# Kernel tuning notes

Measured on AMD Instinct MI355X. Metric: run time of the kernel, lower is better.

## Reference

```python
import jax, jax.numpy as jnp
from jax import lax
import numpy as np

PATCH = 8


def setup_inputs() -> dict:
    key = jax.random.key(0)
    ks = jax.random.split(key, 6)
    B, C, H, W = 8, 128, 256, 256
    half = C // 2
    x = jax.random.normal(ks[0], (B, C, H, W), dtype=jnp.float32)
    # nn.Parameter(torch.randn(...)) -> unit normal real spectral filter
    fft_filt = jax.random.normal(ks[1], (C, PATCH, PATCH // 2 + 1), dtype=jnp.float32)
    w_in = jax.random.normal(ks[2], (C, C), dtype=jnp.float32) * 0.05
    w_before = jax.random.normal(ks[3], (half, half), dtype=jnp.float32) * 0.05
    w_dw = jax.random.normal(ks[4], (half, 1, 3, 3), dtype=jnp.float32) * 0.05
    w_out = jax.random.normal(ks[5], (C, half), dtype=jnp.float32) * 0.05
    return {"x": x, "fft_filt": fft_filt, "w_in": w_in,
            "w_before": w_before, "w_dw": w_dw, "w_out": w_out}


def reference(x, fft_filt, w_in, w_before, w_dw, w_out):
    B, C, H, W = x.shape
    p = PATCH
    pad_h = (p - H % p) % p
    pad_w = (p - W % p) % p
    xp = jnp.pad(x, ((0, 0), (0, 0), (0, pad_h), (0, pad_w))) if (pad_h or pad_w) else x
    Hp, Wp = H + pad_h, W + pad_w
    h, w = Hp // p, Wp // p

    # project_in: 1x1 conv, no bias
    y = jnp.einsum('bchw,oc->bohw', xp, w_in)

    # b c (h p1) (w p2) -> b h w c p1 p2
    yp = y.reshape(B, C, h, p, w, p).transpose(0, 2, 4, 1, 3, 5)
    yf = jnp.fft.rfft2(yp)                      # complex, last-two-axes FFT of 8x8 patches
    yf = yf * fft_filt                          # real filter broadcast over (b,h,w)
    yi = jnp.fft.irfft2(yf, s=(p, p))
    # b h w c p1 p2 -> b c (h p1) (w p2)
    y = yi.transpose(0, 3, 1, 4, 2, 5).reshape(B, C, Hp, Wp)

    # chunk + gated GELU (torch default gelu = exact erf)
    x1, x2 = jnp.split(y, 2, axis=1)
    g = jax.nn.gelu(x1, approximate=False) * x2

    # before_dwconv: 1x1 conv on half channels
    g = jnp.einsum('bchw,oc->bohw', g, w_before)
    # depthwise 3x3, padding 1
    g = lax.conv_general_dilated(g, w_dw, window_strides=(1, 1), padding='SAME',
                                 feature_group_count=C // 2,
                                 dimension_numbers=('NCHW', 'OIHW', 'NCHW'))
    # project_out: 1x1 conv half -> dim
    out = jnp.einsum('bchw,oc->bohw', g, w_out)
    out = out[:, :, :H, :W]
    return out + x
```

## Files before the change

### kernel.cpp

```cpp
#include <hip/hip_runtime.h>
#include <math.h>
#include <stdint.h>

#define BB 8
#define CC 128
#define HH 256
#define WW 256
#define PLANE (HH * WW)
#define YSTR 68

typedef __attribute__((ext_vector_type(8))) short short8;
typedef __attribute__((ext_vector_type(4))) float f32x4;
typedef __attribute__((ext_vector_type(2))) int i32x2;

__device__ __forceinline__ unsigned short f2bf(float f) {
  unsigned u = __float_as_uint(f);
  u += 0x7FFFu + ((u >> 16) & 1u);
  return (unsigned short)(u >> 16);
}
__device__ __forceinline__ float bf2f(unsigned short h) {
  return __uint_as_float(((unsigned)h) << 16);
}

__device__ __forceinline__ i32x2 tr16(uint32_t addr) {
  i32x2 d;
  asm volatile("ds_read_b64_tr_b16 %0, %1" : "=v"(d) : "v"(addr));
  return d;
}
__device__ __forceinline__ short8 mk8(i32x2 a, i32x2 b) {
  union { i32x2 d[2]; short8 s; } u;
  u.d[0] = a; u.d[1] = b;
  return u.s;
}

__global__ __launch_bounds__(256) void prep_kernel(
    const float* __restrict__ filt, const float* __restrict__ w_in,
    const float* __restrict__ w_before, const float* __restrict__ w_out,
    float* __restrict__ kkt, unsigned short* __restrict__ w_in_h,
    unsigned short* __restrict__ w_in_l,
    unsigned short* __restrict__ w_before_h,
    unsigned short* __restrict__ w_before_l, float* __restrict__ w_out_t) {
  int idx = blockIdx.x * 256 + threadIdx.x;
  if (idx < 8192) {
    int c = idx >> 6;
    int un = idx & 63;
    int u = un >> 3, n = un & 7;
    const float cs8[8] = {1.f,  0.70710678118654752f,  0.f, -0.70710678118654752f,
                          -1.f, -0.70710678118654752f, 0.f, 0.70710678118654752f};
    float s = 0.f;
#pragma unroll
    for (int p = 0; p < 8; ++p) {
#pragma unroll
      for (int q = 0; q < 5; ++q) {
        float m = (q == 0 || q == 4) ? 1.f : 2.f;
        s += m * filt[(c * 8 + p) * 5 + q] * cs8[(p * u + q * n) & 7];
      }
    }
    kkt[un * 128 + c] = s * (1.f / 64.f);
  } else if (idx < 24576) {
    int j = idx - 8192;
    float f = w_in[j];
    unsigned short h = f2bf(f);
    w_in_h[j] = h;
    w_in_l[j] = f2bf(f - bf2f(h));
  } else if (idx < 28672) {
    int j = idx - 24576;
    float f = w_before[j];
    unsigned short h = f2bf(f);
    w_before_h[j] = h;
    w_before_l[j] = f2bf(f - bf2f(h));
  } else if (idx < 36864) {
    int j = idx - 28672;
    int o = j >> 6, c = j & 63;
    w_out_t[c * 128 + o] = w_out[o * 64 + c];
  }
}

__global__ __launch_bounds__(256) void fused1_kernel(
    const float* __restrict__ x, const unsigned short* __restrict__ w_in_h,
    const unsigned short* __restrict__ w_in_l,
    const unsigned short* __restrict__ w_before_h,
    const unsigned short* __restrict__ w_before_l,
    const float* __restrict__ kkt, float* __restrict__ g2) {
  __shared__ __align__(16) char smem[51200];
  unsigned short* xh = (unsigned short*)smem;
  unsigned short* xl = (unsigned short*)(smem + 16384);
  float* yb = (float*)smem;
  unsigned short* gh = (unsigned short*)(smem + 34816);
  unsigned short* gl = (unsigned short*)(smem + 43008);

  int bid = blockIdx.x;
  int b = bid >> 10;
  int py = (bid >> 5) & 31;
  int pxb = bid & 31;
  int h0 = py * 8, w0 = pxb * 8;
  int t = threadIdx.x;
  const float* xb = x + (size_t)b * CC * PLANE;

#pragma unroll
  for (int it = 0; it < 4; ++it) {
    int oc = t + it * 256;
    int c = oc >> 3, ph = oc & 7;
    const float* src = xb + (size_t)c * PLANE + (size_t)(h0 + ph) * WW + w0;
    float4 v0 = *(const float4*)src;
    float4 v1 = *(const float4*)(src + 4);
    float v[8] = {v0.x, v0.y, v0.z, v0.w, v1.x, v1.y, v1.z, v1.w};
    unsigned hu[4], lu[4];
#pragma unroll
    for (int q = 0; q < 4; ++q) {
      unsigned short ha = f2bf(v[2 * q]), hb = f2bf(v[2 * q + 1]);
      unsigned short la = f2bf(v[2 * q] - bf2f(ha));
      unsigned short lb = f2bf(v[2 * q + 1] - bf2f(hb));
      hu[q] = (unsigned)ha | ((unsigned)hb << 16);
      lu[q] = (unsigned)la | ((unsigned)lb << 16);
    }
    int ks = c >> 5, wc = c & 31;
    int blk = (wc >> 2) & 1, sg = wc >> 3, jj = wc & 3;
    int nt = ph >> 1, colh = ph & 1;
    int e = ((ks * 4 + nt) * 2 + blk) * 256 + (sg * 4 + jj) * 16 + colh * 8;
    *(uint4*)(xh + e) = make_uint4(hu[0], hu[1], hu[2], hu[3]);
    *(uint4*)(xl + e) = make_uint4(lu[0], lu[1], lu[2], lu[3]);
  }
  __syncthreads();

  int l = t & 63;
  int wv = t >> 6;
  int l15 = l & 15, l4 = l >> 4;
  uint32_t trbase =
      (uint32_t)(uintptr_t)smem + (uint32_t)(l15 * 2 + l4 * 128);

  f32x4 zero4 = {0.f, 0.f, 0.f, 0.f};
  f32x4 acc[2][4];
#pragma unroll
  for (int mt = 0; mt < 2; ++mt)
#pragma unroll
    for (int nt = 0; nt < 4; ++nt) acc[mt][nt] = zero4;

#pragma unroll
  for (int ks = 0; ks < 4; ++ks) {
    short8 ah[2], al[2];
#pragma unroll
    for (int mt = 0; mt < 2; ++mt) {
      int o = wv * 32 + mt * 16 + l15;
      ah[mt] = *(const short8*)(w_in_h + o * 128 + ks * 32 + l4 * 8);
      al[mt] = *(const short8*)(w_in_l + o * 128 + ks * 32 + l4 * 8);
    }
#pragma unroll
    for (int nt = 0; nt < 4; ++nt) {
      uint32_t base = trbase + (uint32_t)((ks * 4 + nt) * 1024);
      i32x2 h0v = tr16(base);
      i32x2 h1v = tr16(base + 512);
      i32x2 l0v = tr16(base + 16384);
      i32x2 l1v = tr16(base + 16384 + 512);
      asm volatile("s_waitcnt lgkmcnt(0)" ::: "memory");
      __builtin_amdgcn_sched_barrier(0);
      short8 bh = mk8(h0v, h1v);
      short8 bl = mk8(l0v, l1v);
#pragma unroll
      for (int mt = 0; mt < 2; ++mt) {
        acc[mt][nt] = __builtin_amdgcn_mfma_f32_16x16x32_bf16(
            ah[mt], bh, acc[mt][nt], 0, 0, 0);
        acc[mt][nt] = __builtin_amdgcn_mfma_f32_16x16x32_bf16(
            ah[mt], bl, acc[mt][nt], 0, 0, 0);
        acc[mt][nt] = __builtin_amdgcn_mfma_f32_16x16x32_bf16(
            al[mt], bh, acc[mt][nt], 0, 0, 0);
      }
    }
  }
  __syncthreads();

#pragma unroll
  for (int mt = 0; mt < 2; ++mt)
#pragma unroll
    for (int nt = 0; nt < 4; ++nt)
#pragma unroll
      for (int r = 0; r < 4; ++r) {
        int o = wv * 32 + mt * 16 + l4 * 4 + r;
        yb[o * YSTR + nt * 16 + l15] = acc[mt][nt][r];
      }
  __syncthreads();

  int ob = t >> 3;
  int pb = t & 7;
  float acc2[4][8];
#pragma unroll
  for (int i = 0; i < 4; ++i)
#pragma unroll
    for (int j = 0; j < 8; ++j) acc2[i][j] = 0.f;

#pragma unroll
  for (int s = 0; s < 8; ++s) {
    int r = (pb - s) & 7;
    float yr[4][8];
#pragma unroll
    for (int i = 0; i < 4; ++i) {
      const float* p = yb + (ob * 4 + i) * YSTR + r * 8;
      float4 v0 = *(const float4*)p;
      float4 v1 = *(const float4*)(p + 4);
      yr[i][0] = v0.x; yr[i][1] = v0.y; yr[i][2] = v0.z; yr[i][3] = v0.w;
      yr[i][4] = v1.x; yr[i][5] = v1.y; yr[i][6] = v1.z; yr[i][7] = v1.w;
    }
#pragma unroll
    for (int tt = 0; tt < 8; ++tt) {
      float4 kv = *(const float4*)(kkt + (s * 8 + tt) * 128 + ob * 4);
      float ka[4] = {kv.x, kv.y, kv.z, kv.w};
#pragma unroll
      for (int i = 0; i < 4; ++i)
#pragma unroll
        for (int j = 0; j < 8; ++j)
          acc2[i][j] += ka[i] * yr[i][(j - tt) & 7];
    }
  }
  __syncthreads();

#pragma unroll
  for (int i = 0; i < 4; ++i) {
    float* dst = yb + (ob * 4 + i) * YSTR + pb * 8;
    *(float4*)dst = make_float4(acc2[i][0], acc2[i][1], acc2[i][2], acc2[i][3]);
    *(float4*)(dst + 4) =
        make_float4(acc2[i][4], acc2[i][5], acc2[i][6], acc2[i][7]);
  }
  __syncthreads();

#pragma unroll
  for (int it = 0; it < 2; ++it) {
    int oc = t + it * 256;
    int c = oc >> 3, ocl = oc & 7;
    const float* pa = yb + c * YSTR + ocl * 8;
    const float* pg = yb + (c + 64) * YSTR + ocl * 8;
    float4 a0 = *(const float4*)pa, a1 = *(const float4*)(pa + 4);
    float4 g0 = *(const float4*)pg, g1 = *(const float4*)(pg + 4);
    float av[8] = {a0.x, a0.y, a0.z, a0.w, a1.x, a1.y, a1.z, a1.w};
    float gv[8] = {g0.x, g0.y, g0.z, g0.w, g1.x, g1.y, g1.z, g1.w};
    unsigned hu[4], lu[4];
#pragma unroll
    for (int q = 0; q < 4; ++q) {
      float r0, r1;
      {
        float a = av[2 * q];
        r0 = 0.5f * a * (1.f + erff(a * 0.70710678118654752f)) * gv[2 * q];
      }
      {
        float a = av[2 * q + 1];
        r1 = 0.5f * a * (1.f + erff(a * 0.70710678118654752f)) * gv[2 * q + 1];
      }
      unsigned short ha = f2bf(r0), hb = f2bf(r1);
      unsigned short la = f2bf(r0 - bf2f(ha)), lb = f2bf(r1 - bf2f(hb));
      hu[q] = (unsigned)ha | ((unsigned)hb << 16);
      lu[q] = (unsigned)la | ((unsigned)lb << 16);
    }
    int ks = c >> 5, wc = c & 31;
    int blk = (wc >> 2) & 1, sg = wc >> 3, jj = wc & 3;
    int nt = ocl >> 1, colh = ocl & 1;
    int e = ((ks * 4 + nt) * 2 + blk) * 256 + (sg * 4 + jj) * 16 + colh * 8;
    *(uint4*)(gh + e) = make_uint4(hu[0], hu[1], hu[2], hu[3]);
    *(uint4*)(gl + e) = make_uint4(lu[0], lu[1], lu[2], lu[3]);
  }
  __syncthreads();

  f32x4 accd[4];
#pragma unroll
  for (int nt = 0; nt < 4; ++nt) accd[nt] = zero4;

  uint32_t gtrbase = (uint32_t)(uintptr_t)smem + 34816u +
                     (uint32_t)(l15 * 2 + l4 * 128);
#pragma unroll
  for (int ks = 0; ks < 2; ++ks) {
    int o = wv * 16 + l15;
    short8 wbh = *(const short8*)(w_before_h + o * 64 + ks * 32 + l4 * 8);
    short8 wbl = *(const short8*)(w_before_l + o * 64 + ks * 32 + l4 * 8);
#pragma unroll
    for (int nt = 0; nt < 4; ++nt) {
      uint32_t base = gtrbase + (uint32_t)((ks * 4 + nt) * 1024);
      i32x2 h0v = tr16(base);
      i32x2 h1v = tr16(base + 512);
      i32x2 l0v = tr16(base + 8192);
      i32x2 l1v = tr16(base + 8192 + 512);
      asm volatile("s_waitcnt lgkmcnt(0)" ::: "memory");
      __builtin_amdgcn_sched_barrier(0);
      short8 bh = mk8(h0v, h1v);
      short8 bl = mk8(l0v, l1v);
      accd[nt] =
          __builtin_amdgcn_mfma_f32_16x16x32_bf16(wbh, bh, accd[nt], 0, 0, 0);
      accd[nt] =
          __builtin_amdgcn_mfma_f32_16x16x32_bf16(wbh, bl, accd[nt], 0, 0, 0);
      accd[nt] =
          __builtin_amdgcn_mfma_f32_16x16x32_bf16(wbl, bh, accd[nt], 0, 0, 0);
    }
  }
#pragma unroll
  for (int nt = 0; nt < 4; ++nt)
#pragma unroll
    for (int r = 0; r < 4; ++r) {
      int o = wv * 16 + l4 * 4 + r;
      yb[o * YSTR + nt * 16 + l15] = accd[nt][r];
    }
  __syncthreads();

#pragma unroll
  for (int it = 0; it < 2; ++it) {
    int oc = t + it * 256;
    int o = oc >> 3, ocl = oc & 7;
    const float* p = yb + o * YSTR + ocl * 8;
    float4 v0 = *(const float4*)p;
    float4 v1 = *(const float4*)(p + 4);
    float* dst = g2 + (size_t)b * 64 * PLANE + (size_t)o * PLANE +
                 (size_t)(h0 + ocl) * WW + w0;
    *(float4*)dst = v0;
    *(float4*)(dst + 4) = v1;
  }
}

__global__ __launch_bounds__(256) void dwconv_kernel(
    const float* __restrict__ g2, const float* __restrict__ w_dw,
    float* __restrict__ dout) {
  int wseg = blockIdx.x;
  int hseg = blockIdx.y;
  int bc = blockIdx.z;
  int c = bc & 63;
  const float* src = g2 + (size_t)bc * PLANE;
  float* dst = dout + (size_t)bc * PLANE;
  __shared__ float tile[34][66];
  int w0 = wseg * 64, h0 = hseg * 32;
  int t = threadIdx.x;
  for (int f = t; f < 34 * 66; f += 256) {
    int r = f / 66, cl = f - r * 66;
    int hh = h0 + r - 1, ww = w0 + cl - 1;
    float v = 0.f;
    if (hh >= 0 && hh < HH && ww >= 0 && ww < WW) v = src[hh * WW + ww];
    tile[r][cl] = v;
  }
  float k9[9];
#pragma unroll
  for (int i = 0; i < 9; ++i) k9[i] = w_dw[c * 9 + i];
  __syncthreads();
  int cl = t & 63;
#pragma unroll
  for (int rep = 0; rep < 8; ++rep) {
    int r = rep * 4 + (t >> 6);
    float s = 0.f;
#pragma unroll
    for (int i = 0; i < 3; ++i)
#pragma unroll
      for (int j = 0; j < 3; ++j) s += k9[i * 3 + j] * tile[r + i][cl + j];
    dst[(size_t)(h0 + r) * WW + w0 + cl] = s;
  }
}

__global__ __launch_bounds__(256) void mixout_kernel(
    const float* __restrict__ d, const float* __restrict__ w_out_t,
    const float* __restrict__ x, float* __restrict__ out) {
  int bid = blockIdx.x;
  int wseg = bid & 3;
  int hh = (bid >> 2) & 255;
  int b = bid >> 10;
  __shared__ float ds[64 * 64];
  int t = threadIdx.x;
  const float* dbase = d + (size_t)b * 64 * PLANE + (size_t)hh * WW + wseg * 64;
#pragma unroll
  for (int i = 0; i < 4; ++i) {
    int f = t + 256 * i;
    int c = f >> 4, k4 = f & 15;
    *(float4*)(ds + c * 64 + k4 * 4) =
        *(const float4*)(dbase + (size_t)c * PLANE + k4 * 4);
  }
  __syncthreads();

  int og = __builtin_amdgcn_readfirstlane(t >> 6);
  int pix = t & 63;
  float acc[32];
#pragma unroll
  for (int i = 0; i < 32; ++i) acc[i] = 0.f;

  const float* wt = w_out_t + og * 32;
#pragma unroll 2
  for (int c = 0; c < 64; ++c) {
    float xv = ds[c * 64 + pix];
#pragma unroll
    for (int i = 0; i < 32; ++i) acc[i] += wt[c * 128 + i] * xv;
  }

  size_t pbase =
      (size_t)b * CC * PLANE + (size_t)hh * WW + (size_t)wseg * 64 + pix;
#pragma unroll
  for (int i = 0; i < 32; ++i) {
    int o = og * 32 + i;
    out[pbase + (size_t)o * PLANE] = acc[i] + x[pbase + (size_t)o * PLANE];
  }
}

extern "C" void kernel_launch(void* const* d_in, const int* in_sizes, int n_in,
                              void* d_out, int out_size, void* d_ws,
                              size_t ws_size, hipStream_t stream) {
  const float* x = (const float*)d_in[0];
  const float* fft_filt = (const float*)d_in[1];
  const float* w_in = (const float*)d_in[2];
  const float* w_before = (const float*)d_in[3];
  const float* w_dw = (const float*)d_in[4];
  const float* w_out = (const float*)d_in[5];
  float* out = (float*)d_out;

  char* ws = (char*)d_ws;
  float* kkt = (float*)ws;
  float* w_out_t = kkt + 8192;
  unsigned short* w_in_h = (unsigned short*)(w_out_t + 8192);
  unsigned short* w_in_l = w_in_h + 16384;
  unsigned short* w_before_h = w_in_l + 16384;
  unsigned short* w_before_l = w_before_h + 4096;
  float* g2 = (float*)(ws + (1 << 20));
  float* dbuf = g2 + (size_t)BB * 64 * PLANE;

  hipLaunchKernelGGL(prep_kernel, dim3(144), dim3(256), 0, stream, fft_filt,
                     w_in, w_before, w_out, kkt, w_in_h, w_in_l, w_before_h,
                     w_before_l, w_out_t);
  hipLaunchKernelGGL(fused1_kernel, dim3(8192), dim3(256), 0, stream, x,
                     w_in_h, w_in_l, w_before_h, w_before_l, kkt, g2);
  hipLaunchKernelGGL(dwconv_kernel, dim3(4, 8, 512), dim3(256), 0, stream, g2,
                     w_dw, dbuf);
  hipLaunchKernelGGL(mixout_kernel, dim3(8192), dim3(256), 0, stream, dbuf,
                     w_out_t, x, out);
}
```

Measured before the change: 1.176 ms.

## Shrink fused1 LDS footprint, prefetch transposed LDS reads, remap block order

Reuses the y buffer region for the gated-GELU bf16 operands so shared memory per block drops from 51200 to 34816 bytes, and adds a launch bound of 4 blocks per CU to raise occupancy. The kkt layout and channel-to-thread mapping change so the spectral-filter stage reads strided channel rows, and the GEGLU results are written in two halves around a barrier to avoid overwriting live data. The ds_read_tr loads in both MFMA loops are software-pipelined one n-tile ahead with partial lgkmcnt waits. Block IDs are remapped so consecutive blocks span different batches. The cost is extra register pressure from the prefetch buffers under the tighter launch bound, and a more intricate LDS aliasing scheme.

```diff
diff --git a/kernel.cpp b/kernel.cpp
--- a/kernel.cpp
+++ b/kernel.cpp
@@ -56,7 +56,7 @@
         s += m * filt[(c * 8 + p) * 5 + q] * cs8[(p * u + q * n) & 7];
       }
     }
-    kkt[un * 128 + c] = s * (1.f / 64.f);
+    kkt[un * 128 + (c & 31) * 4 + (c >> 5)] = s * (1.f / 64.f);
   } else if (idx < 24576) {
     int j = idx - 8192;
     float f = w_in[j];
@@ -76,20 +76,42 @@
   }
 }
 
-__global__ __launch_bounds__(256) void fused1_kernel(
+__device__ __forceinline__ void geglu8(const float* pa, const float* pg,
+                                       uint4& hu, uint4& lu) {
+  float4 a0 = *(const float4*)pa, a1 = *(const float4*)(pa + 4);
+  float4 g0 = *(const float4*)pg, g1 = *(const float4*)(pg + 4);
+  float av[8] = {a0.x, a0.y, a0.z, a0.w, a1.x, a1.y, a1.z, a1.w};
+  float gv[8] = {g0.x, g0.y, g0.z, g0.w, g1.x, g1.y, g1.z, g1.w};
+  unsigned h[4], l[4];
+#pragma unroll
+  for (int q = 0; q < 4; ++q) {
+    float a0s = av[2 * q];
+    float r0 = 0.5f * a0s * (1.f + erff(a0s * 0.70710678118654752f)) * gv[2 * q];
+    float a1s = av[2 * q + 1];
+    float r1 =
+        0.5f * a1s * (1.f + erff(a1s * 0.70710678118654752f)) * gv[2 * q + 1];
+    unsigned short ha = f2bf(r0), hb = f2bf(r1);
+    unsigned short la = f2bf(r0 - bf2f(ha)), lb = f2bf(r1 - bf2f(hb));
+    h[q] = (unsigned)ha | ((unsigned)hb << 16);
+    l[q] = (unsigned)la | ((unsigned)lb << 16);
+  }
+  hu = make_uint4(h[0], h[1], h[2], h[3]);
+  lu = make_uint4(l[0], l[1], l[2], l[3]);
+}
+
+__global__ __launch_bounds__(256, 4) void fused1_kernel(
     const float* __restrict__ x, const unsigned short* __restrict__ w_in_h,
     const unsigned short* __restrict__ w_in_l,
     const unsigned short* __restrict__ w_before_h,
     const unsigned short* __restrict__ w_before_l,
     const float* __restrict__ kkt, float* __restrict__ g2) {
-  __shared__ __align__(16) char smem[51200];
+  __shared__ __align__(16) char smem[34816];
   unsigned short* xh = (unsigned short*)smem;
   unsigned short* xl = (unsigned short*)(smem + 16384);
   float* yb = (float*)smem;
-  unsigned short* gh = (unsigned short*)(smem + 34816);
-  unsigned short* gl = (unsigned short*)(smem + 43008);
-
-  int bid = blockIdx.x;
+
+  int orig = blockIdx.x;
+  int bid = ((orig & 7) << 10) | (orig >> 3);
   int b = bid >> 10;
   int py = (bid >> 5) & 31;
   int pxb = bid & 31;
@@ -126,8 +148,7 @@
   int l = t & 63;
   int wv = t >> 6;
   int l15 = l & 15, l4 = l >> 4;
-  uint32_t trbase =
-      (uint32_t)(uintptr_t)smem + (uint32_t)(l15 * 2 + l4 * 128);
+  uint32_t trbase = (uint32_t)(uintptr_t)smem + (uint32_t)(l15 * 2 + l4 * 128);
 
   f32x4 zero4 = {0.f, 0.f, 0.f, 0.f};
   f32x4 acc[2][4];
@@ -145,17 +166,27 @@
       ah[mt] = *(const short8*)(w_in_h + o * 128 + ks * 32 + l4 * 8);
       al[mt] = *(const short8*)(w_in_l + o * 128 + ks * 32 + l4 * 8);
     }
+    uint32_t b0 = trbase + (uint32_t)(ks * 4096);
+    i32x2 c0, c1, c2, c3, n0, n1, n2, n3;
+    c0 = tr16(b0);
+    c1 = tr16(b0 + 512);
+    c2 = tr16(b0 + 16384);
+    c3 = tr16(b0 + 16896);
 #pragma unroll
     for (int nt = 0; nt < 4; ++nt) {
-      uint32_t base = trbase + (uint32_t)((ks * 4 + nt) * 1024);
-      i32x2 h0v = tr16(base);
-      i32x2 h1v = tr16(base + 512);
-      i32x2 l0v = tr16(base + 16384);
-      i32x2 l1v = tr16(base + 16384 + 512);
-      asm volatile("s_waitcnt lgkmcnt(0)" ::: "memory");
+      if (nt < 3) {
+        uint32_t bn = b0 + (uint32_t)((nt + 1) * 1024);
+        n0 = tr16(bn);
+        n1 = tr16(bn + 512);
+        n2 = tr16(bn + 16384);
+        n3 = tr16(bn + 16896);
+        asm volatile("s_waitcnt lgkmcnt(4)" ::: "memory");
+      } else {
+        asm volatile("s_waitcnt lgkmcnt(0)" ::: "memory");
+      }
       __builtin_amdgcn_sched_barrier(0);
-      short8 bh = mk8(h0v, h1v);
-      short8 bl = mk8(l0v, l1v);
+      short8 bh = mk8(c0, c1);
+      short8 bl = mk8(c2, c3);
 #pragma unroll
       for (int mt = 0; mt < 2; ++mt) {
         acc[mt][nt] = __builtin_amdgcn_mfma_f32_16x16x32_bf16(
@@ -165,6 +196,7 @@
         acc[mt][nt] = __builtin_amdgcn_mfma_f32_16x16x32_bf16(
             al[mt], bh, acc[mt][nt], 0, 0, 0);
       }
+      c0 = n0; c1 = n1; c2 = n2; c3 = n3;
     }
   }
   __syncthreads();
@@ -194,7 +226,7 @@
     float yr[4][8];
 #pragma unroll
     for (int i = 0; i < 4; ++i) {
-      const float* p = yb + (ob * 4 + i) * YSTR + r * 8;
+      const float* p = yb + (ob + 32 * i) * YSTR + r * 8;
       float4 v0 = *(const float4*)p;
       float4 v1 = *(const float4*)(p + 4);
       yr[i][0] = v0.x; yr[i][1] = v0.y; yr[i][2] = v0.z; yr[i][3] = v0.w;
@@ -215,77 +247,75 @@
 
 #pragma unroll
   for (int i = 0; i < 4; ++i) {
-    float* dst = yb + (ob * 4 + i) * YSTR + pb * 8;
+    float* dst = yb + (ob + 32 * i) * YSTR + pb * 8;
     *(float4*)dst = make_float4(acc2[i][0], acc2[i][1], acc2[i][2], acc2[i][3]);
     *(float4*)(dst + 4) =
         make_float4(acc2[i][4], acc2[i][5], acc2[i][6], acc2[i][7]);
   }
   __syncthreads();
 
-#pragma unroll
-  for (int it = 0; it < 2; ++it) {
-    int oc = t + it * 256;
-    int c = oc >> 3, ocl = oc & 7;
-    const float* pa = yb + c * YSTR + ocl * 8;
-    const float* pg = yb + (c + 64) * YSTR + ocl * 8;
-    float4 a0 = *(const float4*)pa, a1 = *(const float4*)(pa + 4);
-    float4 g0 = *(const float4*)pg, g1 = *(const float4*)(pg + 4);
-    float av[8] = {a0.x, a0.y, a0.z, a0.w, a1.x, a1.y, a1.z, a1.w};
-    float gv[8] = {g0.x, g0.y, g0.z, g0.w, g1.x, g1.y, g1.z, g1.w};
-    unsigned hu[4], lu[4];
-#pragma unroll
-    for (int q = 0; q < 4; ++q) {
-      float r0, r1;
-      {
-        float a = av[2 * q];
-        r0 = 0.5f * a * (1.f + erff(a * 0.70710678118654752f)) * gv[2 * q];
+  int cc = t >> 3;
+  int ocl = t & 7;
+  uint4 hu1, lu1;
+  geglu8(yb + cc * YSTR + ocl * 8, yb + (cc + 64) * YSTR + ocl * 8, hu1, lu1);
+  __syncthreads();
+  int blkc = (cc >> 2) & 1, sgc = cc >> 3, jjc = cc & 3;
+  int ntc = ocl >> 1, colhc = ocl & 1;
+  int eG = (ntc * 2 + blkc) * 256 + (sgc * 4 + jjc) * 16 + colhc * 8;
+  *(uint4*)(smem + 2 * eG) = hu1;
+  *(uint4*)(smem + 4096 + 2 * eG) = lu1;
+  {
+    int c2 = cc + 32;
+    uint4 hu2, lu2;
+    geglu8(yb + c2 * YSTR + ocl * 8, yb + (c2 + 64) * YSTR + ocl * 8, hu2, lu2);
+    *(uint4*)(smem + 17408 + 2 * eG) = hu2;
+    *(uint4*)(smem + 21504 + 2 * eG) = lu2;
+  }
+  __syncthreads();
+
+  f32x4 accd[4];
+#pragma unroll
+  for (int nt = 0; nt < 4; ++nt) accd[nt] = zero4;
+
+  int od = wv * 16 + l15;
+  short8 wbh0 = *(const short8*)(w_before_h + od * 64 + l4 * 8);
+  short8 wbl0 = *(const short8*)(w_before_l + od * 64 + l4 * 8);
+  short8 wbh1 = *(const short8*)(w_before_h + od * 64 + 32 + l4 * 8);
+  short8 wbl1 = *(const short8*)(w_before_l + od * 64 + 32 + l4 * 8);
+
+  uint32_t gb0 = (uint32_t)(uintptr_t)smem + (uint32_t)(l15 * 2 + l4 * 128);
+#pragma unroll
+  for (int ks = 0; ks < 2; ++ks) {
+    uint32_t rb = gb0 + (ks ? 17408u : 0u);
+    short8 wbh = ks ? wbh1 : wbh0;
+    short8 wbl = ks ? wbl1 : wbl0;
+    i32x2 c0, c1, c2, c3, n0, n1, n2, n3;
+    c0 = tr16(rb);
+    c1 = tr16(rb + 512);
+    c2 = tr16(rb + 4096);
+    c3 = tr16(rb + 4608);
+#pragma unroll
+    for (int nt = 0; nt < 4; ++nt) {
+      if (nt < 3) {
+        uint32_t bn = rb + (uint32_t)((nt + 1) * 1024);
+        n0 = tr16(bn);
+        n1 = tr16(bn + 512);
+        n2 = tr16(bn + 4096);
+        n3 = tr16(bn + 4608);
+        asm volatile("s_waitcnt lgkmcnt(4)" ::: "memory");
+      } else {
+        asm volatile("s_waitcnt lgkmcnt(0)" ::: "memory");
       }
-      {
-        float a = av[2 * q + 1];
-        r1 = 0.5f * a * (1.f + erff(a * 0.70710678118654752f)) * gv[2 * q + 1];
-      }
-      unsigned short ha = f2bf(r0), hb = f2bf(r1);
-      unsigned short la = f2bf(r0 - bf2f(ha)), lb = f2bf(r1 - bf2f(hb));
-      hu[q] = (unsigned)ha | ((unsigned)hb << 16);
-      lu[q] = (unsigned)la | ((unsigned)lb << 16);
-    }
-    int ks = c >> 5, wc = c & 31;
-    int blk = (wc >> 2) & 1, sg = wc >> 3, jj = wc & 3;
-    int nt = ocl >> 1, colh = ocl & 1;
-    int e = ((ks * 4 + nt) * 2 + blk) * 256 + (sg * 4 + jj) * 16 + colh * 8;
-    *(uint4*)(gh + e) = make_uint4(hu[0], hu[1], hu[2], hu[3]);
-    *(uint4*)(gl + e) = make_uint4(lu[0], lu[1], lu[2], lu[3]);
-  }
-  __syncthreads();
-
-  f32x4 accd[4];
-#pragma unroll
-  for (int nt = 0; nt < 4; ++nt) accd[nt] = zero4;
-
-  uint32_t gtrbase = (uint32_t)(uintptr_t)smem + 34816u +
-                     (uint32_t)(l15 * 2 + l4 * 128);
-#pragma unroll
-  for (int ks = 0; ks < 2; ++ks) {
-    int o = wv * 16 + l15;
-    short8 wbh = *(const short8*)(w_before_h + o * 64 + ks * 32 + l4 * 8);
-    short8 wbl = *(const short8*)(w_before_l + o * 64 + ks * 32 + l4 * 8);
-#pragma unroll
-    for (int nt = 0; nt < 4; ++nt) {
-      uint32_t base = gtrbase + (uint32_t)((ks * 4 + nt) * 1024);
-      i32x2 h0v = tr16(base);
-      i32x2 h1v = tr16(base + 512);
-      i32x2 l0v = tr16(base + 8192);
-      i32x2 l1v = tr16(base + 8192 + 512);
-      asm volatile("s_waitcnt lgkmcnt(0)" ::: "memory");
       __builtin_amdgcn_sched_barrier(0);
-      short8 bh = mk8(h0v, h1v);
-      short8 bl = mk8(l0v, l1v);
+      short8 bh = mk8(c0, c1);
+      short8 bl = mk8(c2, c3);
       accd[nt] =
           __builtin_amdgcn_mfma_f32_16x16x32_bf16(wbh, bh, accd[nt], 0, 0, 0);
       accd[nt] =
           __builtin_amdgcn_mfma_f32_16x16x32_bf16(wbh, bl, accd[nt], 0, 0, 0);
       accd[nt] =
           __builtin_amdgcn_mfma_f32_16x16x32_bf16(wbl, bh, accd[nt], 0, 0, 0);
+      c0 = n0; c1 = n1; c2 = n2; c3 = n3;
     }
   }
 #pragma unroll
@@ -293,19 +323,21 @@
 #pragma unroll
     for (int r = 0; r < 4; ++r) {
       int o = wv * 16 + l4 * 4 + r;
-      yb[o * YSTR + nt * 16 + l15] = accd[nt][r];
+      int rr = (o < 32) ? (32 + o) : (64 + o);
+      yb[rr * YSTR + nt * 16 + l15] = accd[nt][r];
     }
   __syncthreads();
 
 #pragma unroll
   for (int it = 0; it < 2; ++it) {
     int oc = t + it * 256;
-    int o = oc >> 3, ocl = oc & 7;
-    const float* p = yb + o * YSTR + ocl * 8;
+    int o = oc >> 3, ph = oc & 7;
+    int rr = (o < 32) ? (32 + o) : (64 + o);
+    const float* p = yb + rr * YSTR + ph * 8;
     float4 v0 = *(const float4*)p;
     float4 v1 = *(const float4*)(p + 4);
     float* dst = g2 + (size_t)b * 64 * PLANE + (size_t)o * PLANE +
-                 (size_t)(h0 + ocl) * WW + w0;
+                 (size_t)(h0 + ph) * WW + w0;
     *(float4*)dst = v0;
     *(float4*)(dst + 4) = v1;
   }
```

After: 1.309 ms. 1.11x slower.
